# Performance work log

Measured on AMD Instinct MI355X. Metric: run time of the kernel, lower is better.

Reference implementation:

```python
import jax, jax.numpy as jnp
import numpy as np

NUM_CODES = 512
CODE_DIM = 64
BETA = 0.25  # commitment_cost


def setup_inputs() -> dict:
    key = jax.random.key(0)
    k1, k2 = jax.random.split(key)
    B, D, H, T = 32, CODE_DIM, 16, 256
    z_e = jax.random.normal(k1, (B, D, H, T), dtype=jnp.float32)
    embed = jax.random.normal(k2, (NUM_CODES, D), dtype=jnp.float32)
    # F.normalize(embed, dim=1) * init_scale (init_scale=1.0)
    embed = embed / jnp.clip(jnp.linalg.norm(embed, axis=1, keepdims=True), 1e-12)
    return {"z_e": z_e, "embedding": embed}


def reference(z_e, embedding):
    B, D, H, T = z_e.shape
    K = embedding.shape[0]
    # (B,D,H,T) -> (N,D)
    flat_z_e = jnp.transpose(z_e, (0, 2, 3, 1)).reshape(-1, D)

    # squared L2 distances: ||z||^2 + ||e||^2 - 2 z.e  -> (N,K)
    z_sq = jnp.sum(flat_z_e * flat_z_e, axis=1, keepdims=True)          # (N,1)
    e_sq = jnp.sum(embedding * embedding, axis=1)[None, :]              # (1,K)
    dot = flat_z_e @ embedding.T                                        # (N,K)
    distances = z_sq + e_sq - 2.0 * dot
    indices = jnp.argmin(distances, axis=1)                             # (N,)

    # nearest-code lookup (same math as onehot @ embedding)
    z_q_flat = embedding[indices]                                       # (N,D)
    z_q = jnp.transpose(z_q_flat.reshape(B, H, T, D), (0, 3, 1, 2))     # (B,D,H,T)

    # straight-through estimator
    z_q_st = z_e + jax.lax.stop_gradient(z_q - z_e)

    # commitment loss: beta * mse(stop_grad(z_e), z_q)
    commitment = BETA * jnp.mean((jax.lax.stop_gradient(z_e) - z_q) ** 2)

    # usage statistics
    N = flat_z_e.shape[0]
    counts = jnp.zeros((K,), dtype=jnp.float32).at[indices].add(1.0)
    avg_probs = counts / N
    eps = 1e-12
    entropy = -jnp.sum(avg_probs * jnp.log(avg_probs + eps))
    perplexity = jnp.exp(entropy)
    usage = jnp.mean((avg_probs > 0).astype(jnp.float32))

    return (z_q_st, commitment, indices.reshape(B, H, T), perplexity, usage)
```

## Files before the change

### kernel.cpp

```cpp
#include <hip/hip_runtime.h>

#define BB 32
#define DD 64
#define HH 16
#define TT 256
#define KK 512
#define NN (BB*HH*TT)
#define HT (HH*TT)
#define DHT (DD*HT)
#define ZQ_SIZE (BB*DD*HH*TT)
#define COMMIT_OFF ZQ_SIZE
#define IDX_OFF (ZQ_SIZE+1)
#define PPL_OFF (IDX_OFF+NN)
#define USE_OFF (PPL_OFF+1)

#define CNT_OFF    0
#define CPART_OFF  512
#define CDELTA_OFF 2560
#define RC_OFF     2561
#define RLIST_OFF  2562
#define RMAX       16384
#define EBH_OFF    36864
#define EBL_OFF    53248

#define MARGIN_A 1.5e-3f

using bf16x8 = __attribute__((ext_vector_type(8))) short;
using f32x4  = __attribute__((ext_vector_type(4))) float;

__device__ __forceinline__ unsigned bf16_rne(float x) {
    unsigned u = __float_as_uint(x);
    return (u + 0x7FFFu + ((u >> 16) & 1u)) >> 16;
}
__device__ __forceinline__ bf16x8 bc(uint4 v) { return __builtin_bit_cast(bf16x8, v); }
__device__ __forceinline__ float pick4(float a0, float a1, float a2, float a3, int i) {
    float x = (i & 1) ? a1 : a0;
    float y = (i & 1) ? a3 : a2;
    return (i & 2) ? y : x;
}

__global__ void vq_init(const float* __restrict__ emb, float* __restrict__ ws) {
    const int tid = threadIdx.x, blk = blockIdx.x;
    if (blk == 0) {
        ws[CNT_OFF + tid] = 0.0f;
        ws[CNT_OFF + 256 + tid] = 0.0f;
        if (tid == 0) { ws[CDELTA_OFF] = 0.0f; ((int*)ws)[RC_OFF] = 0; }
    }
    const int k  = blk * 16 + (tid >> 4);
    const int d0 = (tid & 15) * 4;
    float4 v = *reinterpret_cast<const float4*>(emb + k * DD + d0);
    unsigned hx = bf16_rne(v.x), hy = bf16_rne(v.y), hz = bf16_rne(v.z), hw = bf16_rne(v.w);
    float lx = v.x - __uint_as_float(hx << 16);
    float ly = v.y - __uint_as_float(hy << 16);
    float lz = v.z - __uint_as_float(hz << 16);
    float lw = v.w - __uint_as_float(hw << 16);
    uint2 hi, lo;
    hi.x = hx | (hy << 16);            hi.y = hz | (hw << 16);
    lo.x = bf16_rne(lx) | (bf16_rne(ly) << 16);
    lo.y = bf16_rne(lz) | (bf16_rne(lw) << 16);
    reinterpret_cast<uint2*>(ws + EBH_OFF)[(k * DD + d0) >> 2] = hi;
    reinterpret_cast<uint2*>(ws + EBL_OFF)[(k * DD + d0) >> 2] = lo;
}

__global__ __launch_bounds__(256, 2) void vq_screen(
    const float* __restrict__ z_e, const float* __restrict__ emb,
    float* __restrict__ ws, float* __restrict__ out_zq, float* __restrict__ out_idx)
{
    __shared__ uint4 sh[2][2304];
    __shared__ int hist[KK];

    const int tid  = threadIdx.x;
    const int lane = tid & 63;
    const int col  = lane & 15;
    const int q    = lane >> 4;
    const int W    = (blockIdx.x * 256 + tid) >> 6;
    const int base_tok = W * 64;

    hist[tid] = 0; hist[tid + 256] = 0;

    const uint4* ebh4 = reinterpret_cast<const uint4*>(ws + EBH_OFF);
    const uint4* ebl4 = reinterpret_cast<const uint4*>(ws + EBL_OFF);

    bf16x8 ah[4][2], al[4][2];
    float zp[4];
#pragma unroll
    for (int s = 0; s < 4; ++s) {
        zp[s] = 0.0f;
        const int n = base_tok + s * 16 + col;
        const size_t zoff = (size_t)(n >> 12) * DHT + (size_t)((n >> 8) & 15) * 256 + (size_t)(n & 255);
#pragma unroll
        for (int kf = 0; kf < 2; ++kf) {
            const int d0 = kf * 32 + q * 8;
            unsigned hu[4], lu[4];
#pragma unroll
            for (int jj = 0; jj < 4; ++jj) {
                float z0 = z_e[zoff + (size_t)(d0 + 2*jj + 0) * HT];
                float z1 = z_e[zoff + (size_t)(d0 + 2*jj + 1) * HT];
                zp[s] = fmaf(z0, z0, zp[s]);
                zp[s] = fmaf(z1, z1, zp[s]);
                unsigned h0 = bf16_rne(z0), h1 = bf16_rne(z1);
                float l0 = z0 - __uint_as_float(h0 << 16);
                float l1 = z1 - __uint_as_float(h1 << 16);
                hu[jj] = h0 | (h1 << 16);
                lu[jj] = bf16_rne(l0) | (bf16_rne(l1) << 16);
            }
            ah[s][kf] = bc(make_uint4(hu[0], hu[1], hu[2], hu[3]));
            al[s][kf] = bc(make_uint4(lu[0], lu[1], lu[2], lu[3]));
        }
    }
#pragma unroll
    for (int s = 0; s < 4; ++s) {
        zp[s] += __shfl_xor(zp[s], 16, 64);
        zp[s] += __shfl_xor(zp[s], 32, 64);
    }

    float m1[4][4], m2[4][4];
#pragma unroll
    for (int s = 0; s < 4; ++s)
#pragma unroll
        for (int r = 0; r < 4; ++r) { m1[s][r] = -3.4e38f; m2[s][r] = -3.4e38f; }

    unsigned ktag = (unsigned)col;
    const int idx0 = col * 9 + q;

#pragma unroll
    for (int p = 0; p < 2; ++p) {
        if (p) __syncthreads();
#pragma unroll
        for (int j = 0; j < 8; ++j) {
            const int local = j * 256 + tid;
            const int c = local >> 3, jj = local & 7;
            sh[0][c * 9 + jj] = ebh4[p * 2048 + local];
            sh[1][c * 9 + jj] = ebl4[p * 2048 + local];
        }
        __syncthreads();

        uint4 nh0 = sh[0][idx0], nh1 = sh[0][idx0 + 4];
        uint4 nl0 = sh[1][idx0], nl1 = sh[1][idx0 + 4];

#pragma unroll 4
        for (int ctl = 0; ctl < 16; ++ctl) {
            bf16x8 bh0 = bc(nh0), bh1 = bc(nh1);
            bf16x8 bl0 = bc(nl0), bl1 = bc(nl1);
            if (ctl < 15) {
                const int ni = idx0 + (ctl + 1) * 144;
                nh0 = sh[0][ni]; nh1 = sh[0][ni + 4];
                nl0 = sh[1][ni]; nl1 = sh[1][ni + 4];
            }
#pragma unroll
            for (int s = 0; s < 4; ++s) {
                f32x4 acc = {0.f, 0.f, 0.f, 0.f};
                acc = __builtin_amdgcn_mfma_f32_16x16x32_bf16(ah[s][0], bh0, acc, 0, 0, 0);
                acc = __builtin_amdgcn_mfma_f32_16x16x32_bf16(ah[s][1], bh1, acc, 0, 0, 0);
                acc = __builtin_amdgcn_mfma_f32_16x16x32_bf16(al[s][0], bh0, acc, 0, 0, 0);
                acc = __builtin_amdgcn_mfma_f32_16x16x32_bf16(al[s][1], bh1, acc, 0, 0, 0);
                acc = __builtin_amdgcn_mfma_f32_16x16x32_bf16(ah[s][0], bl0, acc, 0, 0, 0);
                acc = __builtin_amdgcn_mfma_f32_16x16x32_bf16(ah[s][1], bl1, acc, 0, 0, 0);
#pragma unroll
                for (int r = 0; r < 4; ++r) {
                    float pk = __uint_as_float((__float_as_uint(acc[r]) & 0xFFFFFE00u) | ktag);
                    m2[s][r] = __builtin_amdgcn_fmed3f(pk, m1[s][r], m2[s][r]);
                    m1[s][r] = fmaxf(m1[s][r], pk);
                }
            }
            ktag += 16u;
        }
    }

#pragma unroll
    for (int msk = 1; msk <= 8; msk <<= 1) {
#pragma unroll
        for (int s = 0; s < 4; ++s)
#pragma unroll
            for (int r = 0; r < 4; ++r) {
                float o1 = __shfl_xor(m1[s][r], msk, 64);
                float o2 = __shfl_xor(m2[s][r], msk, 64);
                m2[s][r] = __builtin_amdgcn_fmed3f(m1[s][r], o1, fmaxf(m2[s][r], o2));
                m1[s][r] = fmaxf(m1[s][r], o1);
            }
    }

    const int s0 = col >> 2, r0 = col & 3;
    const int token = base_tok + s0 * 16 + q * 4 + r0;

    float m1v, m2v;
    {
        float a = pick4(m1[0][0], m1[0][1], m1[0][2], m1[0][3], r0);
        float b = pick4(m1[1][0], m1[1][1], m1[1][2], m1[1][3], r0);
        float c = pick4(m1[2][0], m1[2][1], m1[2][2], m1[2][3], r0);
        float d = pick4(m1[3][0], m1[3][1], m1[3][2], m1[3][3], r0);
        m1v = pick4(a, b, c, d, s0);
        a = pick4(m2[0][0], m2[0][1], m2[0][2], m2[0][3], r0);
        b = pick4(m2[1][0], m2[1][1], m2[1][2], m2[1][3], r0);
        c = pick4(m2[2][0], m2[2][1], m2[2][2], m2[2][3], r0);
        d = pick4(m2[3][0], m2[3][1], m2[3][2], m2[3][3], s0 * 0 + r0);
        m2v = pick4(a, b, c, d, s0);
    }
    const int c0 = q * 4 + r0;
    float z0s = __shfl(zp[0], c0, 64);
    float z1s = __shfl(zp[1], c0, 64);
    float z2s = __shfl(zp[2], c0, 64);
    float z3s = __shfl(zp[3], c0, 64);
    const float zsqv = pick4(z0s, z1s, z2s, z3s, s0);

    const int k_sel = (int)(__float_as_uint(m1v) & 511u);
    const float dminA = fmaf(-2.0f, m1v, zsqv + 1.0f);

    out_idx[token] = (float)k_sel;
    if (m1v - m2v < MARGIN_A) {
        int* rc = (int*)ws + RC_OFF;
        int pp = atomicAdd(rc, 1);
        if (pp < RMAX) {
            int* rl = (int*)ws + RLIST_OFF;
            rl[2 * pp] = token;
            rl[2 * pp + 1] = (int)__float_as_uint(dminA);
        }
    }
    atomicAdd(&hist[k_sel], 1);

    float csum = dminA;
#pragma unroll
    for (int off = 32; off > 0; off >>= 1) csum += __shfl_down(csum, off, 64);
    if (lane == 0) ws[CPART_OFF + W] = csum;

    {
        const int b = token >> 12, h = (token >> 8) & 15, t = token & 255;
        const size_t zb = (size_t)b * DHT + (size_t)h * TT + (size_t)t;
        const float4* er = reinterpret_cast<const float4*>(emb + (size_t)k_sel * DD);
#pragma unroll
        for (int i = 0; i < 16; ++i) {
            float4 v = er[i];
            out_zq[zb + (size_t)(4*i+0) * HT] = v.x;
            out_zq[zb + (size_t)(4*i+1) * HT] = v.y;
            out_zq[zb + (size_t)(4*i+2) * HT] = v.z;
            out_zq[zb + (size_t)(4*i+3) * HT] = v.w;
        }
    }

    __syncthreads();
    int c = hist[tid];       if (c) atomicAdd(ws + CNT_OFF + tid,       (float)c);
    c     = hist[tid + 256]; if (c) atomicAdd(ws + CNT_OFF + tid + 256, (float)c);
}

__global__ void vq_rescue(const float* __restrict__ z_e, const float* __restrict__ emb,
                          float* __restrict__ ws, float* __restrict__ out_zq,
                          float* __restrict__ out_idx)
{
    __shared__ float lz[DD];
    __shared__ float sd[512];
    __shared__ int   si[512];
    const int tid = threadIdx.x;
    int cnt = ((const int*)ws)[RC_OFF];
    if (cnt > RMAX) cnt = RMAX;
    const int* rl = (const int*)ws + RLIST_OFF;

    for (int it = blockIdx.x; it < cnt; it += gridDim.x) {
        const int n = rl[2 * it];
        const float dminA = __uint_as_float((unsigned)rl[2 * it + 1]);
        const int b = n >> 12, h = (n >> 8) & 15, t = n & 255;
        const size_t zoff = (size_t)b * DHT + (size_t)h * 256 + (size_t)t;
        __syncthreads();
        if (tid < DD) lz[tid] = z_e[zoff + (size_t)tid * HT];
        __syncthreads();
        const float4* er = reinterpret_cast<const float4*>(emb + (size_t)tid * DD);
        float a0 = 0.f, a1 = 0.f, a2 = 0.f, a3 = 0.f;
#pragma unroll
        for (int i = 0; i < 16; ++i) {
            float4 e4 = er[i];
            float d0 = lz[4*i+0] - e4.x; a0 = fmaf(d0, d0, a0);
            float d1 = lz[4*i+1] - e4.y; a1 = fmaf(d1, d1, a1);
            float d2 = lz[4*i+2] - e4.z; a2 = fmaf(d2, d2, a2);
            float d3 = lz[4*i+3] - e4.w; a3 = fmaf(d3, d3, a3);
        }
        sd[tid] = (a0 + a1) + (a2 + a3);
        si[tid] = tid;
        __syncthreads();
        for (int off = 256; off > 0; off >>= 1) {
            if (tid < off) {
                float d2 = sd[tid + off]; int j2 = si[tid + off];
                if (d2 < sd[tid] || (d2 == sd[tid] && j2 < si[tid])) { sd[tid] = d2; si[tid] = j2; }
            }
            __syncthreads();
        }
        const int   k_new = si[0];
        const float d_new = sd[0];
        const int   k_old = (int)out_idx[n];
        if (tid == 0) {
            atomicAdd(ws + CDELTA_OFF, d_new - dminA);
            if (k_new != k_old) {
                out_idx[n] = (float)k_new;
                atomicAdd(ws + CNT_OFF + k_old, -1.0f);
                atomicAdd(ws + CNT_OFF + k_new,  1.0f);
            }
        }
        if (k_new != k_old && tid < DD)
            out_zq[zoff + (size_t)tid * HT] = emb[(size_t)k_new * DD + tid];
        __syncthreads();
    }
}

__global__ void vq_stats(const float* __restrict__ ws, float* __restrict__ out) {
    __shared__ float s_ent[KK];
    __shared__ int   s_used[KK];
    __shared__ float s_com[KK];
    const int k = threadIdx.x;
    const float c = ws[CNT_OFF + k];
    const float p = c * (1.0f / (float)NN);
    s_ent[k]  = p * logf(p + 1e-12f);
    s_used[k] = (p > 0.0f) ? 1 : 0;
    float cs = ws[CPART_OFF + k] + ws[CPART_OFF + 512 + k]
             + ws[CPART_OFF + 1024 + k] + ws[CPART_OFF + 1536 + k];
    s_com[k] = cs;
    __syncthreads();
    for (int off = 256; off > 0; off >>= 1) {
        if (k < off) {
            s_ent[k]  += s_ent[k + off];
            s_used[k] += s_used[k + off];
            s_com[k]  += s_com[k + off];
        }
        __syncthreads();
    }
    if (k == 0) {
        out[COMMIT_OFF] = 0.25f * (s_com[0] + ws[CDELTA_OFF]) / (float)ZQ_SIZE;
        out[PPL_OFF]    = expf(-s_ent[0]);
        out[USE_OFF]    = (float)s_used[0] / (float)KK;
    }
}

extern "C" void kernel_launch(void* const* d_in, const int* in_sizes, int n_in,
                              void* d_out, int out_size, void* d_ws, size_t ws_size,
                              hipStream_t stream) {
    const float* z_e = (const float*)d_in[0];
    const float* emb = (const float*)d_in[1];
    float* out = (float*)d_out;
    float* ws  = (float*)d_ws;

    float* out_idx = out + IDX_OFF;

    vq_init<<<32, 256, 0, stream>>>(emb, ws);
    vq_screen<<<512, 256, 0, stream>>>(z_e, emb, ws, out, out_idx);
    vq_rescue<<<256, 512, 0, stream>>>(z_e, emb, ws, out, out_idx);
    vq_stats<<<1, 512, 0, stream>>>(ws, out);
}
```

Baseline: 133.1 us.

## Use single-wave screen blocks reading codebook from L2, fuse stats into rescue

The screen kernel now runs one 64-thread wave per block and reads a pre-swizzled hi/lo bf16 codebook directly from global memory with register double-buffering. This drops the shared-memory staging, its barriers and the per-block histogram. Histogram counts are now atomically added to global memory per token, and the bf16 hi/lo split uses truncation instead of round-to-nearest. The stats kernel is folded into the rescue kernel through a last-block-done counter, which removes one launch. The trade is more global atomics and L2 codebook traffic, plus a slightly different hi/lo split that may change how tight the screening margin is.

```diff
diff --git a/kernel.cpp b/kernel.cpp
--- a/kernel.cpp
+++ b/kernel.cpp
@@ -18,20 +18,16 @@
 #define CPART_OFF  512
 #define CDELTA_OFF 2560
 #define RC_OFF     2561
-#define RLIST_OFF  2562
+#define DONE_OFF   2562
+#define RLIST_OFF  2564
 #define RMAX       16384
-#define EBH_OFF    36864
-#define EBL_OFF    53248
+#define EB_OFF     36864
 
 #define MARGIN_A 1.5e-3f
 
 using bf16x8 = __attribute__((ext_vector_type(8))) short;
 using f32x4  = __attribute__((ext_vector_type(4))) float;
 
-__device__ __forceinline__ unsigned bf16_rne(float x) {
-    unsigned u = __float_as_uint(x);
-    return (u + 0x7FFFu + ((u >> 16) & 1u)) >> 16;
-}
 __device__ __forceinline__ bf16x8 bc(uint4 v) { return __builtin_bit_cast(bf16x8, v); }
 __device__ __forceinline__ float pick4(float a0, float a1, float a2, float a3, int i) {
     float x = (i & 1) ? a1 : a0;
@@ -44,42 +40,42 @@
     if (blk == 0) {
         ws[CNT_OFF + tid] = 0.0f;
         ws[CNT_OFF + 256 + tid] = 0.0f;
-        if (tid == 0) { ws[CDELTA_OFF] = 0.0f; ((int*)ws)[RC_OFF] = 0; }
+        if (tid == 0) {
+            ws[CDELTA_OFF] = 0.0f;
+            ((int*)ws)[RC_OFF] = 0;
+            ((int*)ws)[DONE_OFF] = 0;
+        }
     }
     const int k  = blk * 16 + (tid >> 4);
     const int d0 = (tid & 15) * 4;
     float4 v = *reinterpret_cast<const float4*>(emb + k * DD + d0);
-    unsigned hx = bf16_rne(v.x), hy = bf16_rne(v.y), hz = bf16_rne(v.z), hw = bf16_rne(v.w);
-    float lx = v.x - __uint_as_float(hx << 16);
-    float ly = v.y - __uint_as_float(hy << 16);
-    float lz = v.z - __uint_as_float(hz << 16);
-    float lw = v.w - __uint_as_float(hw << 16);
+    unsigned ux = __float_as_uint(v.x), uy = __float_as_uint(v.y);
+    unsigned uz = __float_as_uint(v.z), uw = __float_as_uint(v.w);
+    unsigned hx = ux & 0xFFFF0000u, hy = uy & 0xFFFF0000u;
+    unsigned hz = uz & 0xFFFF0000u, hw = uw & 0xFFFF0000u;
+    float lx = v.x - __uint_as_float(hx), ly = v.y - __uint_as_float(hy);
+    float lz = v.z - __uint_as_float(hz), lw = v.w - __uint_as_float(hw);
     uint2 hi, lo;
-    hi.x = hx | (hy << 16);            hi.y = hz | (hw << 16);
-    lo.x = bf16_rne(lx) | (bf16_rne(ly) << 16);
-    lo.y = bf16_rne(lz) | (bf16_rne(lw) << 16);
-    reinterpret_cast<uint2*>(ws + EBH_OFF)[(k * DD + d0) >> 2] = hi;
-    reinterpret_cast<uint2*>(ws + EBL_OFF)[(k * DD + d0) >> 2] = lo;
-}
-
-__global__ __launch_bounds__(256, 2) void vq_screen(
+    hi.x = (ux >> 16) | hy;
+    hi.y = (uz >> 16) | hw;
+    lo.x = (__float_as_uint(lx) >> 16) | (__float_as_uint(ly) & 0xFFFF0000u);
+    lo.y = (__float_as_uint(lz) >> 16) | (__float_as_uint(lw) & 0xFFFF0000u);
+    const int ctl = k >> 4, colc = k & 15;
+    uint2* dst = reinterpret_cast<uint2*>(ws + EB_OFF);
+    const int u2 = ctl * 512 + colc * 16 + (d0 >> 2);
+    dst[u2]       = hi;
+    dst[u2 + 256] = lo;
+}
+
+__global__ __launch_bounds__(64, 2) void vq_screen(
     const float* __restrict__ z_e, const float* __restrict__ emb,
     float* __restrict__ ws, float* __restrict__ out_zq, float* __restrict__ out_idx)
 {
-    __shared__ uint4 sh[2][2304];
-    __shared__ int hist[KK];
-
-    const int tid  = threadIdx.x;
-    const int lane = tid & 63;
+    const int lane = threadIdx.x;
     const int col  = lane & 15;
     const int q    = lane >> 4;
-    const int W    = (blockIdx.x * 256 + tid) >> 6;
+    const int W    = blockIdx.x;
     const int base_tok = W * 64;
-
-    hist[tid] = 0; hist[tid + 256] = 0;
-
-    const uint4* ebh4 = reinterpret_cast<const uint4*>(ws + EBH_OFF);
-    const uint4* ebl4 = reinterpret_cast<const uint4*>(ws + EBL_OFF);
 
     bf16x8 ah[4][2], al[4][2];
     float zp[4];
@@ -98,11 +94,12 @@
                 float z1 = z_e[zoff + (size_t)(d0 + 2*jj + 1) * HT];
                 zp[s] = fmaf(z0, z0, zp[s]);
                 zp[s] = fmaf(z1, z1, zp[s]);
-                unsigned h0 = bf16_rne(z0), h1 = bf16_rne(z1);
-                float l0 = z0 - __uint_as_float(h0 << 16);
-                float l1 = z1 - __uint_as_float(h1 << 16);
-                hu[jj] = h0 | (h1 << 16);
-                lu[jj] = bf16_rne(l0) | (bf16_rne(l1) << 16);
+                unsigned u0 = __float_as_uint(z0), u1 = __float_as_uint(z1);
+                unsigned h0 = u0 & 0xFFFF0000u,   h1 = u1 & 0xFFFF0000u;
+                float l0 = z0 - __uint_as_float(h0);
+                float l1 = z1 - __uint_as_float(h1);
+                hu[jj] = (u0 >> 16) | h1;
+                lu[jj] = (__float_as_uint(l0) >> 16) | (__float_as_uint(l1) & 0xFFFF0000u);
             }
             ah[s][kf] = bc(make_uint4(hu[0], hu[1], hu[2], hu[3]));
             al[s][kf] = bc(make_uint4(lu[0], lu[1], lu[2], lu[3]));
@@ -121,50 +118,40 @@
         for (int r = 0; r < 4; ++r) { m1[s][r] = -3.4e38f; m2[s][r] = -3.4e38f; }
 
     unsigned ktag = (unsigned)col;
-    const int idx0 = col * 9 + q;
-
-#pragma unroll
-    for (int p = 0; p < 2; ++p) {
-        if (p) __syncthreads();
-#pragma unroll
-        for (int j = 0; j < 8; ++j) {
-            const int local = j * 256 + tid;
-            const int c = local >> 3, jj = local & 7;
-            sh[0][c * 9 + jj] = ebh4[p * 2048 + local];
-            sh[1][c * 9 + jj] = ebl4[p * 2048 + local];
-        }
-        __syncthreads();
-
-        uint4 nh0 = sh[0][idx0], nh1 = sh[0][idx0 + 4];
-        uint4 nl0 = sh[1][idx0], nl1 = sh[1][idx0 + 4];
-
-#pragma unroll 4
-        for (int ctl = 0; ctl < 16; ++ctl) {
-            bf16x8 bh0 = bc(nh0), bh1 = bc(nh1);
-            bf16x8 bl0 = bc(nl0), bl1 = bc(nl1);
-            if (ctl < 15) {
-                const int ni = idx0 + (ctl + 1) * 144;
-                nh0 = sh[0][ni]; nh1 = sh[0][ni + 4];
-                nl0 = sh[1][ni]; nl1 = sh[1][ni + 4];
-            }
-#pragma unroll
-            for (int s = 0; s < 4; ++s) {
-                f32x4 acc = {0.f, 0.f, 0.f, 0.f};
-                acc = __builtin_amdgcn_mfma_f32_16x16x32_bf16(ah[s][0], bh0, acc, 0, 0, 0);
-                acc = __builtin_amdgcn_mfma_f32_16x16x32_bf16(ah[s][1], bh1, acc, 0, 0, 0);
-                acc = __builtin_amdgcn_mfma_f32_16x16x32_bf16(al[s][0], bh0, acc, 0, 0, 0);
-                acc = __builtin_amdgcn_mfma_f32_16x16x32_bf16(al[s][1], bh1, acc, 0, 0, 0);
-                acc = __builtin_amdgcn_mfma_f32_16x16x32_bf16(ah[s][0], bl0, acc, 0, 0, 0);
-                acc = __builtin_amdgcn_mfma_f32_16x16x32_bf16(ah[s][1], bl1, acc, 0, 0, 0);
-#pragma unroll
-                for (int r = 0; r < 4; ++r) {
-                    float pk = __uint_as_float((__float_as_uint(acc[r]) & 0xFFFFFE00u) | ktag);
-                    m2[s][r] = __builtin_amdgcn_fmed3f(pk, m1[s][r], m2[s][r]);
-                    m1[s][r] = fmaxf(m1[s][r], pk);
-                }
-            }
-            ktag += 16u;
-        }
+
+    const uint4* eb = reinterpret_cast<const uint4*>(ws + EB_OFF);
+    const uint4* pb = eb + col * 8 + q;
+
+    uint4 Bh0[2], Bh1[2], Bl0[2], Bl1[2];
+    Bh0[0] = pb[0];   Bh1[0] = pb[4];   Bl0[0] = pb[128]; Bl1[0] = pb[132];
+    Bh0[1] = pb[256]; Bh1[1] = pb[260]; Bl0[1] = pb[384]; Bl1[1] = pb[388];
+
+#pragma unroll
+    for (int ctl = 0; ctl < 32; ++ctl) {
+        const int pr = ctl & 1;
+        bf16x8 bh0 = bc(Bh0[pr]), bh1 = bc(Bh1[pr]);
+        bf16x8 bl0 = bc(Bl0[pr]), bl1 = bc(Bl1[pr]);
+        if (ctl < 30) {
+            const uint4* pp = pb + (ctl + 2) * 256;
+            Bh0[pr] = pp[0]; Bh1[pr] = pp[4]; Bl0[pr] = pp[128]; Bl1[pr] = pp[132];
+        }
+#pragma unroll
+        for (int s = 0; s < 4; ++s) {
+            f32x4 acc = {0.f, 0.f, 0.f, 0.f};
+            acc = __builtin_amdgcn_mfma_f32_16x16x32_bf16(ah[s][0], bh0, acc, 0, 0, 0);
+            acc = __builtin_amdgcn_mfma_f32_16x16x32_bf16(ah[s][1], bh1, acc, 0, 0, 0);
+            acc = __builtin_amdgcn_mfma_f32_16x16x32_bf16(al[s][0], bh0, acc, 0, 0, 0);
+            acc = __builtin_amdgcn_mfma_f32_16x16x32_bf16(al[s][1], bh1, acc, 0, 0, 0);
+            acc = __builtin_amdgcn_mfma_f32_16x16x32_bf16(ah[s][0], bl0, acc, 0, 0, 0);
+            acc = __builtin_amdgcn_mfma_f32_16x16x32_bf16(ah[s][1], bl1, acc, 0, 0, 0);
+#pragma unroll
+            for (int r = 0; r < 4; ++r) {
+                float pk = __uint_as_float((__float_as_uint(acc[r]) & 0xFFFFFE00u) | ktag);
+                m2[s][r] = __builtin_amdgcn_fmed3f(pk, m1[s][r], m2[s][r]);
+                m1[s][r] = fmaxf(m1[s][r], pk);
+            }
+        }
+        ktag += 16u;
     }
 
 #pragma unroll
@@ -193,7 +180,7 @@
         a = pick4(m2[0][0], m2[0][1], m2[0][2], m2[0][3], r0);
         b = pick4(m2[1][0], m2[1][1], m2[1][2], m2[1][3], r0);
         c = pick4(m2[2][0], m2[2][1], m2[2][2], m2[2][3], r0);
-        d = pick4(m2[3][0], m2[3][1], m2[3][2], m2[3][3], s0 * 0 + r0);
+        d = pick4(m2[3][0], m2[3][1], m2[3][2], m2[3][3], r0);
         m2v = pick4(a, b, c, d, s0);
     }
     const int c0 = q * 4 + r0;
@@ -216,7 +203,7 @@
             rl[2 * pp + 1] = (int)__float_as_uint(dminA);
         }
     }
-    atomicAdd(&hist[k_sel], 1);
+    atomicAdd(ws + CNT_OFF + k_sel, 1.0f);
 
     float csum = dminA;
 #pragma unroll
@@ -236,19 +223,18 @@
             out_zq[zb + (size_t)(4*i+3) * HT] = v.w;
         }
     }
-
-    __syncthreads();
-    int c = hist[tid];       if (c) atomicAdd(ws + CNT_OFF + tid,       (float)c);
-    c     = hist[tid + 256]; if (c) atomicAdd(ws + CNT_OFF + tid + 256, (float)c);
-}
-
-__global__ void vq_rescue(const float* __restrict__ z_e, const float* __restrict__ emb,
-                          float* __restrict__ ws, float* __restrict__ out_zq,
-                          float* __restrict__ out_idx)
+}
+
+__global__ void vq_rescue_stats(const float* __restrict__ z_e, const float* __restrict__ emb,
+                                float* __restrict__ ws, float* __restrict__ out,
+                                float* __restrict__ out_idx)
 {
     __shared__ float lz[DD];
     __shared__ float sd[512];
     __shared__ int   si[512];
+    __shared__ float s_com[512];
+    __shared__ int   amlast;
+    float* out_zq = out;
     const int tid = threadIdx.x;
     int cnt = ((const int*)ws)[RC_OFF];
     if (cnt > RMAX) cnt = RMAX;
@@ -257,8 +243,8 @@
     for (int it = blockIdx.x; it < cnt; it += gridDim.x) {
         const int n = rl[2 * it];
         const float dminA = __uint_as_float((unsigned)rl[2 * it + 1]);
-        const int b = n >> 12, h = (n >> 8) & 15, t = n & 255;
-        const size_t zoff = (size_t)b * DHT + (size_t)h * 256 + (size_t)t;
+        const int b = n >> 12, h = (n >> 8) & 15;
+        const size_t zoff = (size_t)b * DHT + (size_t)h * 256 + (size_t)(n & 255);
         __syncthreads();
         if (tid < DD) lz[tid] = z_e[zoff + (size_t)tid * HT];
         __syncthreads();
@@ -297,33 +283,36 @@
             out_zq[zoff + (size_t)tid * HT] = emb[(size_t)k_new * DD + tid];
         __syncthreads();
     }
-}
-
-__global__ void vq_stats(const float* __restrict__ ws, float* __restrict__ out) {
-    __shared__ float s_ent[KK];
-    __shared__ int   s_used[KK];
-    __shared__ float s_com[KK];
-    const int k = threadIdx.x;
-    const float c = ws[CNT_OFF + k];
+
+    __threadfence();
+    if (tid == 0) {
+        int d = atomicAdd((int*)ws + DONE_OFF, 1);
+        amlast = (d == (int)gridDim.x - 1) ? 1 : 0;
+    }
+    __syncthreads();
+    if (!amlast) return;
+
+    const int k = tid;
+    const float c = __hip_atomic_load(ws + CNT_OFF + k, __ATOMIC_RELAXED, __HIP_MEMORY_SCOPE_AGENT);
     const float p = c * (1.0f / (float)NN);
-    s_ent[k]  = p * logf(p + 1e-12f);
-    s_used[k] = (p > 0.0f) ? 1 : 0;
-    float cs = ws[CPART_OFF + k] + ws[CPART_OFF + 512 + k]
+    sd[k]    = p * logf(p + 1e-12f);
+    si[k]    = (p > 0.0f) ? 1 : 0;
+    s_com[k] = ws[CPART_OFF + k] + ws[CPART_OFF + 512 + k]
              + ws[CPART_OFF + 1024 + k] + ws[CPART_OFF + 1536 + k];
-    s_com[k] = cs;
     __syncthreads();
     for (int off = 256; off > 0; off >>= 1) {
         if (k < off) {
-            s_ent[k]  += s_ent[k + off];
-            s_used[k] += s_used[k + off];
-            s_com[k]  += s_com[k + off];
+            sd[k]    += sd[k + off];
+            si[k]    += si[k + off];
+            s_com[k] += s_com[k + off];
         }
         __syncthreads();
     }
     if (k == 0) {
-        out[COMMIT_OFF] = 0.25f * (s_com[0] + ws[CDELTA_OFF]) / (float)ZQ_SIZE;
-        out[PPL_OFF]    = expf(-s_ent[0]);
-        out[USE_OFF]    = (float)s_used[0] / (float)KK;
+        float cdelta = __hip_atomic_load(ws + CDELTA_OFF, __ATOMIC_RELAXED, __HIP_MEMORY_SCOPE_AGENT);
+        out[COMMIT_OFF] = 0.25f * (s_com[0] + cdelta) / (float)ZQ_SIZE;
+        out[PPL_OFF]    = expf(-sd[0]);
+        out[USE_OFF]    = (float)si[0] / (float)KK;
     }
 }
 
@@ -338,7 +327,6 @@
     float* out_idx = out + IDX_OFF;
 
     vq_init<<<32, 256, 0, stream>>>(emb, ws);
-    vq_screen<<<512, 256, 0, stream>>>(z_e, emb, ws, out, out_idx);
-    vq_rescue<<<256, 512, 0, stream>>>(z_e, emb, ws, out, out_idx);
-    vq_stats<<<1, 512, 0, stream>>>(ws, out);
-}
+    vq_screen<<<2048, 64, 0, stream>>>(z_e, emb, ws, out, out_idx);
+    vq_rescue_stats<<<256, 512, 0, stream>>>(z_e, emb, ws, out, out_idx);
+}
```

After: 210.5 us. 58.2% more time.
